# Performance work log

Hardware: AMD Instinct MI355X
Metric: run time of the kernel (lower is better)

Reference implementation:

```python
import jax, jax.numpy as jnp
import numpy as np

N_FFT = 512
HOP = 128
WIN = 512
Q = 0.1
PCT_WIN = 31
FREQ_WIN = 5
TIME_WIN = 9
STRENGTH = 0.35
THRESH = 1.5
TEMP = 0.15
MIN_MASK = 0.08


def _hann_periodic(n):
    # matches torch.hann_window(n) (periodic)
    return (0.5 * (1.0 - jnp.cos(2.0 * jnp.pi * jnp.arange(n) / n))).astype(jnp.float32)


def _stft(x, window):
    # x: (B, L) -> complex (B, F, T); center=True, reflect pad
    pad = N_FFT // 2
    xp = jnp.pad(x, ((0, 0), (pad, pad)), mode='reflect')
    T = 1 + (xp.shape[-1] - N_FFT) // HOP
    idx = (jnp.arange(T) * HOP)[:, None] + jnp.arange(N_FFT)  # (T, n_fft)
    frames = xp[:, idx] * window  # (B, T, n_fft)
    return jnp.fft.rfft(frames, axis=-1).transpose(0, 2, 1)  # (B, F, T)


def _istft(spec, window, length):
    # spec: (B, F, T) complex -> (B, length)
    frames = jnp.fft.irfft(spec.transpose(0, 2, 1), n=N_FFT, axis=-1) * window  # (B,T,n_fft)
    B, T, _ = frames.shape
    total = N_FFT + HOP * (T - 1)
    idx = ((jnp.arange(T) * HOP)[:, None] + jnp.arange(N_FFT)).ravel()
    out = jnp.zeros((B, total), frames.dtype).at[:, idx].add(frames.reshape(B, -1))
    wsq = jnp.zeros((total,), frames.dtype).at[idx].add(
        jnp.broadcast_to(window ** 2, (T, N_FFT)).ravel())
    out = out / jnp.maximum(wsq, 1e-11)
    pad = N_FFT // 2
    return out[:, pad:pad + length]


def _rolling_quantile(mag):
    # mag: (B, F, T); replicate pad + sliding window of PCT_WIN along time
    p = PCT_WIN // 2
    padded = jnp.pad(mag, ((0, 0), (0, 0), (p, p)), mode='edge')
    T = mag.shape[-1]
    windows = jnp.stack([padded[..., i:i + T] for i in range(PCT_WIN)], axis=-1)  # (B,F,T,W)
    return jnp.quantile(windows, Q, axis=-1)


def _avg_pool(x, k, axis):
    # stride-1 avg pool with zero pad k//2, count_include_pad=True (torch default)
    if k <= 1:
        return x
    p = k // 2
    pads = [(0, 0)] * x.ndim
    pads[axis] = (p, p)
    xp = jnp.pad(x, pads)
    n = x.shape[axis]
    acc = 0.0
    for i in range(k):
        sl = [slice(None)] * x.ndim
        sl[axis] = slice(i, i + n)
        acc = acc + xp[tuple(sl)]
    return acc / k


def setup_inputs() -> dict:
    key = jax.random.key(0)
    k1, k2 = jax.random.split(key)
    B, L = 16, 160000
    noisy = jax.random.normal(k1, (B, L), dtype=jnp.float32)
    enhanced = jax.random.normal(k2, (B, L), dtype=jnp.float32)
    return {"noisy": noisy, "enhanced": enhanced}


def reference(noisy, enhanced):
    length = enhanced.shape[-1]
    window = _hann_periodic(WIN)
    e_spec = _stft(enhanced, window)
    n_spec = _stft(noisy, window)
    e_mag = jnp.maximum(jnp.abs(e_spec), 1e-6)
    n_mag = jnp.maximum(jnp.abs(n_spec), 1e-6)
    # mode == 'sg_input_floor': source is the noisy magnitude
    floor = _rolling_quantile(n_mag)
    floor = _avg_pool(floor, FREQ_WIN, axis=-2)
    floor = _avg_pool(floor, TIME_WIN, axis=-1)
    floor = jnp.maximum(floor, 1e-6)
    mask = jax.nn.sigmoid((e_mag - THRESH * floor) / (TEMP * floor + 1e-6))
    final_mask = MIN_MASK + (1.0 - MIN_MASK) * (1.0 - STRENGTH + STRENGTH * mask)
    phase = e_spec / jnp.maximum(jnp.abs(e_spec), 1e-12)  # unit-phase, = polar(1, angle)
    gated_spec = (e_mag * final_mask).astype(jnp.float32) * phase
    return _istft(gated_spec, window, length)
```

## Files before the change

### kernel.cpp

```cpp
#include <hip/hip_runtime.h>
#include <hip/hip_bf16.h>
#include <math.h>

#define BATCH 16
#define LEN   160000
#define NFFT  512
#define HOP   128
#define NT    1251
#define NF    257
#define PADC  256
#define TWO_PI 6.28318530717958647692f
#define P(i) ((i) + ((i) >> 5))
#define FBUF 528
#define GSTR 264

__device__ __forceinline__ int reflect_idx(int j) {
    j = j < 0 ? -j : j;
    j = j >= LEN ? 2*LEN - 2 - j : j;
    return j;
}

__device__ __forceinline__ float hann(int n) {
    return 0.5f - 0.5f * __cosf(TWO_PI * (float)n * (1.0f / 512.0f));
}

__device__ __forceinline__ __hip_bfloat162 pack_bf2(float x, float y) {
    __hip_bfloat162 r; r.x = __float2bfloat16(x); r.y = __float2bfloat16(y); return r;
}
__device__ __forceinline__ float2 unpack_bf2(__hip_bfloat162 v) {
    return make_float2(__bfloat162float(v.x), __bfloat162float(v.y));
}

struct T4 { float m0, m1, m2, m3; };

__device__ __forceinline__ void ins(T4& a, float v) {
    const float x0 = fminf(a.m0, v);  const float c0 = fmaxf(a.m0, v);
    const float x1 = fminf(a.m1, c0); const float c1 = fmaxf(a.m1, c0);
    const float x2 = fminf(a.m2, c1); const float c2 = fmaxf(a.m2, c1);
    const float x3 = fminf(a.m3, c2);
    a.m0 = x0; a.m1 = x1; a.m2 = x2; a.m3 = x3;
}

__device__ __forceinline__ T4 sort4(float a, float b, float c, float d) {
    const float x0 = fminf(a, b), x1 = fmaxf(a, b);
    const float x2 = fminf(c, d), x3 = fmaxf(c, d);
    const float y0 = fminf(x0, x2), y2 = fmaxf(x0, x2);
    const float y1 = fminf(x1, x3), y3 = fmaxf(x1, x3);
    T4 r; r.m0 = y0; r.m1 = fminf(y1, y2); r.m2 = fmaxf(y1, y2); r.m3 = y3;
    return r;
}

__device__ __forceinline__ float merge4_m3(const T4& a, const T4& b) {
    const float l0 = fminf(a.m0, b.m3);
    const float l1 = fminf(a.m1, b.m2);
    const float l2 = fminf(a.m2, b.m1);
    const float l3 = fminf(a.m3, b.m0);
    return fmaxf(fmaxf(l0, l1), fmaxf(l2, l3));
}

__device__ __forceinline__ void dft8(float vr[8], float vi[8], float sign) {
    const float K = 0.70710678118654752f;
    float ar=vr[0]+vr[4], ai=vi[0]+vi[4];
    float br=vr[0]-vr[4], bi=vi[0]-vi[4];
    float cr=vr[2]+vr[6], ci=vi[2]+vi[6];
    float dr=vr[2]-vr[6], di=vi[2]-vi[6];
    float er=vr[1]+vr[5], ei=vi[1]+vi[5];
    float fr=vr[1]-vr[5], fi=vi[1]-vi[5];
    float gr=vr[3]+vr[7], gi=vi[3]+vi[7];
    float hr=vr[3]-vr[7], hi=vi[3]-vi[7];
    const float W4dr = -sign*di, W4di = sign*dr;
    const float W4hr = -sign*hi, W4hi = sign*hr;
    const float E0r=ar+cr, E0i=ai+ci, E2r=ar-cr, E2i=ai-ci;
    const float E1r=br+W4dr, E1i=bi+W4di, E3r=br-W4dr, E3i=bi-W4di;
    const float O0r=er+gr, O0i=ei+gi, O2r=er-gr, O2i=ei-gi;
    const float O1r=fr+W4hr, O1i=fi+W4hi, O3r=fr-W4hr, O3i=fi-W4hi;
    const float T1r = K*(O1r - sign*O1i), T1i = K*(O1i + sign*O1r);
    const float T2r = -sign*O2i,          T2i = sign*O2r;
    const float T3r = K*(-O3r - sign*O3i), T3i = K*(-O3i + sign*O3r);
    vr[0]=E0r+O0r; vi[0]=E0i+O0i;  vr[4]=E0r-O0r; vi[4]=E0i-O0i;
    vr[1]=E1r+T1r; vi[1]=E1i+T1i;  vr[5]=E1r-T1r; vi[5]=E1i-T1i;
    vr[2]=E2r+T2r; vi[2]=E2i+T2i;  vr[6]=E2r-T2r; vi[6]=E2i-T2i;
    vr[3]=E3r+T3r; vi[3]=E3i+T3i;  vr[7]=E3r-T3r; vi[7]=E3i-T3i;
}

template<int NS>
__device__ __forceinline__ void fft_pass(float* R, float* I, int j, float sign) {
    float vr[8], vi[8];
    #pragma unroll
    for (int r = 0; r < 8; ++r) { vr[r] = R[P(j + 64*r)]; vi[r] = I[P(j + 64*r)]; }
    const float th = sign * (TWO_PI / (8.0f * (float)NS)) * (float)(j & (NS - 1));
    float w1r, w1i; __sincosf(th, &w1i, &w1r);
    float wr = w1r, wi = w1i;
    #pragma unroll
    for (int r = 1; r < 8; ++r) {
        const float tr = vr[r]*wr - vi[r]*wi;
        vi[r] = vr[r]*wi + vi[r]*wr; vr[r] = tr;
        const float nwr = wr*w1r - wi*w1i;
        wi = wr*w1i + wi*w1r; wr = nwr;
    }
    dft8(vr, vi, sign);
    const int base = ((j / NS) * (8 * NS)) + (j & (NS - 1));
    #pragma unroll
    for (int r = 0; r < 8; ++r) { R[P(base + r*NS)] = vr[r]; I[P(base + r*NS)] = vi[r]; }
}

__device__ __forceinline__ void fft_pass_last(const float* R, const float* I, int j,
                                              float sign, float vr[8], float vi[8]) {
    #pragma unroll
    for (int r = 0; r < 8; ++r) { vr[r] = R[P(j + 64*r)]; vi[r] = I[P(j + 64*r)]; }
    const float th = sign * (TWO_PI / 512.0f) * (float)j;
    float w1r, w1i; __sincosf(th, &w1i, &w1r);
    float wr = w1r, wi = w1i;
    #pragma unroll
    for (int r = 1; r < 8; ++r) {
        const float tr = vr[r]*wr - vi[r]*wi;
        vi[r] = vr[r]*wi + vi[r]*wr; vr[r] = tr;
        const float nwr = wr*w1r - wi*w1i;
        wi = wr*w1i + wi*w1r; wr = nwr;
    }
    dft8(vr, vi, sign);
}

__global__ __launch_bounds__(256, 6) void stft_kernel(const float* __restrict__ enh,
                                                      const float* __restrict__ noi,
                                                      __hip_bfloat162* __restrict__ e_spec,
                                                      __hip_bfloat16*  __restrict__ n_mag,
                                                      float* __restrict__ out) {
    __shared__ float Ar[4*FBUF], Ai[4*FBUF];
    const int tid = threadIdx.x;
    const int w = tid >> 6, j = tid & 63;
    const int tr_ = blockIdx.x * 4 + w;
    const bool live = tr_ < NT;
    const int t = live ? tr_ : NT - 1;
    const int b = blockIdx.y;
    float* ar = Ar + w*FBUF; float* ai = Ai + w*FBUF;

    {
        const int z = (blockIdx.x << 9) + (tid << 1);
        if (z < LEN) *reinterpret_cast<float2*>(out + (size_t)b * LEN + z) = make_float2(0.0f, 0.0f);
    }

    {
        const int sbase = t * HOP - PADC;
        float vr[8], vi[8];
        if (sbase >= 0 && sbase + NFFT <= LEN) {
            const float* __restrict__ pe = enh + b * LEN + sbase;
            const float* __restrict__ pn = noi + b * LEN + sbase;
            #pragma unroll
            for (int r = 0; r < 8; ++r) {
                const int n = j + 64*r;
                const float wd = hann(n);
                vr[r] = pe[n] * wd;
                vi[r] = pn[n] * wd;
            }
        } else {
            const float* __restrict__ pe = enh + b * LEN;
            const float* __restrict__ pn = noi + b * LEN;
            #pragma unroll
            for (int r = 0; r < 8; ++r) {
                const int n = j + 64*r;
                const int idx = reflect_idx(sbase + n);
                const float wd = hann(n);
                vr[r] = pe[idx] * wd;
                vi[r] = pn[idx] * wd;
            }
        }
        dft8(vr, vi, -1.0f);
        #pragma unroll
        for (int r = 0; r < 8; ++r) { ar[P(8*j + r)] = vr[r]; ai[P(8*j + r)] = vi[r]; }
    }
    fft_pass<8>(ar, ai, j, -1.0f);
    float zr[8], zi[8];
    fft_pass_last(ar, ai, j, -1.0f, zr, zi);

    const int src = (64 - j) & 63;
    float pr[4], pi_[4];
    #pragma unroll
    for (int q = 4; q < 8; ++q) {
        pr[q-4]  = __shfl(zr[q], src);
        pi_[q-4] = __shfl(zi[q], src);
    }
    if (live) {
        const int obase = (b * NT + t) * NF;
        #pragma unroll
        for (int r = 0; r < 4; ++r) {
            const int kk = j + 64*r;
            const float yr = (j == 0) ? zr[(8 - r) & 7] : pr[3 - r];
            const float yi = (j == 0) ? zi[(8 - r) & 7] : pi_[3 - r];
            const float er = 0.5f*(zr[r] + yr), ei = 0.5f*(zi[r] - yi);
            const float nr = 0.5f*(zi[r] + yi), ni = 0.5f*(yr - zr[r]);
            e_spec[obase + kk] = pack_bf2(er, ei);
            n_mag[obase + kk] = __float2bfloat16(fmaxf(sqrtf(nr*nr + ni*ni), 1e-6f));
        }
        if (j == 0) {
            e_spec[obase + 256] = pack_bf2(zr[4], 0.0f);
            n_mag[obase + 256] = __float2bfloat16(fmaxf(fabsf(zi[4]), 1e-6f));
        }
    }
}

__global__ __launch_bounds__(256, 4) void floor_mask_istft_kernel(
        const __hip_bfloat162* __restrict__ g,
        const __hip_bfloat16* __restrict__ n_mag,
        float* __restrict__ out) {
    __shared__ float smem[16 * GSTR];
    __shared__ float fq[16];
    float (*q)[GSTR] = reinterpret_cast<float (*)[GSTR]>(smem);
    float* gr = smem;
    float* gi = smem + 8 * GSTR;

    const int tid = threadIdx.x;
    const int w = tid >> 6, j = tid & 63;
    const int t0 = blockIdx.x * 8, b = blockIdx.y;
    const __hip_bfloat16* __restrict__ pb = n_mag + b * NT * NF;

    {
        const int f = tid;
        float wa[16];
        #pragma unroll
        for (int r = 0; r < 16; ++r) {
            int tr = t0 - 19 + r;
            tr = tr < 0 ? 0 : (tr > NT - 1 ? NT - 1 : tr);
            wa[r] = __bfloat162float(pb[tr * NF + f]);
        }
        T4 s[16];
        s[15].m0 = wa[15]; s[15].m1 = 3.4e38f; s[15].m2 = 3.4e38f; s[15].m3 = 3.4e38f;
        #pragma unroll
        for (int k = 14; k >= 0; --k) { s[k] = s[k+1]; ins(s[k], wa[k]); }
        float wc[15];
        #pragma unroll
        for (int r = 0; r < 15; ++r) {
            int tr = t0 - 3 + r;
            tr = tr < 0 ? 0 : (tr > NT - 1 ? NT - 1 : tr);
            wc[r] = __bfloat162float(pb[tr * NF + f]);
        }
        T4 p = sort4(wc[0], wc[1], wc[2], wc[3]);
        #pragma unroll
        for (int r = 4; r < 15; ++r) ins(p, wc[r]);
        float wb[15];
        #pragma unroll
        for (int r = 0; r < 15; ++r) {
            int tr = t0 + 12 + r;
            tr = tr < 0 ? 0 : (tr > NT - 1 ? NT - 1 : tr);
            wb[r] = __bfloat162float(pb[tr * NF + f]);
        }
        #pragma unroll
        for (int k = 0; k < 16; ++k) {
            q[k][f] = merge4_m3(s[k], p);
            if (k < 15) ins(p, wb[k]);
        }
    }
    if (tid < 16) {
        const int k = tid;
        T4 m; m.m0 = m.m1 = m.m2 = m.m3 = 3.4e38f;
        for (int dt = -15; dt <= 15; ++dt) {
            int tt = t0 - 4 + k + dt;
            tt = tt < 0 ? 0 : (tt > NT - 1 ? NT - 1 : tt);
            ins(m, __bfloat162float(pb[tt * NF + 256]));
        }
        q[k][256] = m.m3;
    }
    __syncthreads();

    float fp[16];
    {
        const int f = tid;
        #pragma unroll
        for (int k = 0; k < 16; ++k) {
            float acc = 0.0f;
            #pragma unroll
            for (int df = -2; df <= 2; ++df) {
                const int ff = f + df;
                if (ff >= 0 && ff < NF) acc += q[k][ff];
            }
            fp[k] = acc * (1.0f / 5.0f);
        }
    }
    if (tid < 16) fq[tid] = (q[tid][254] + q[tid][255] + q[tid][256]) * (1.0f / 5.0f);
    __syncthreads();

    float flv[8];
    {
        #pragma unroll
        for (int k = 0; k < 16; ++k) {
            const int tq = t0 - 4 + k;
            fp[k] = (tq >= 0 && tq < NT) ? fp[k] : 0.0f;
        }
        float acc = 0.0f;
        #pragma unroll
        for (int k = 0; k < 9; ++k) acc += fp[k];
        #pragma unroll
        for (int to = 0; to < 8; ++to) {
            flv[to] = fmaxf(acc * (1.0f / 9.0f), 1e-6f);
            if (to < 7) acc += fp[to + 9] - fp[to];
        }
    }

    {
        const int f = tid;
        #pragma unroll
        for (int ft = 0; ft < 8; ++ft) {
            const int t = t0 + ft;
            float grv = 0.0f, giv = 0.0f;
            if (t < NT) {
                const float fl = flv[ft];
                const float2 e2 = unpack_bf2(g[(b * NT + t) * NF + f]);
                const float a = sqrtf(e2.x * e2.x + e2.y * e2.y);
                const float emag = fmaxf(a, 1e-6f);
                const float xarg = (emag - 1.5f * fl) / (0.15f * fl + 1e-6f);
                const float mask = 1.0f / (1.0f + __expf(-xarg));
                const float fm = 0.08f + 0.92f * (0.65f + 0.35f * mask);
                const float scale = emag * fm / fmaxf(a, 1e-12f);
                grv = e2.x * scale; giv = e2.y * scale;
            }
            gr[ft * GSTR + f] = grv;
            gi[ft * GSTR + f] = giv;
        }
    }
    if (tid < 8) {
        const int ft = tid;
        const int t = t0 + ft;
        float grv = 0.0f, giv = 0.0f;
        if (t < NT) {
            float acc = 0.0f;
            #pragma unroll
            for (int k = 0; k < 9; ++k) {
                const int tq = t0 - 4 + ft + k;
                acc += (tq >= 0 && tq < NT) ? fq[ft + k] : 0.0f;
            }
            const float fl = fmaxf(acc * (1.0f / 9.0f), 1e-6f);
            const float2 e2 = unpack_bf2(g[(b * NT + t) * NF + 256]);
            const float a = sqrtf(e2.x * e2.x + e2.y * e2.y);
            const float emag = fmaxf(a, 1e-6f);
            const float xarg = (emag - 1.5f * fl) / (0.15f * fl + 1e-6f);
            const float mask = 1.0f / (1.0f + __expf(-xarg));
            const float fm = 0.08f + 0.92f * (0.65f + 0.35f * mask);
            const float scale = emag * fm / fmaxf(a, 1e-12f);
            grv = e2.x * scale; giv = e2.y * scale;
        }
        gr[ft * GSTR + 256] = grv;
        gi[ft * GSTR + 256] = giv;
    }
    __syncthreads();

    float* g0r = gr + (2*w) * GSTR;      float* g0i = gi + (2*w) * GSTR;
    float* g1r = gr + (2*w + 1) * GSTR;  float* g1i = gi + (2*w + 1) * GSTR;
    float* ar = g0r;
    float* ai = g0i;

    {
        float vr[8], vi[8];
        #pragma unroll
        for (int r = 0; r < 8; ++r) {
            const int n = j + 64*r;
            float cr, ci;
            if (n <= 256) {
                cr = g0r[n] - g1i[n];
                ci = g0i[n] + g1r[n];
            } else {
                const int m = 512 - n;
                cr = g0r[m] + g1i[m];
                ci = g1r[m] - g0i[m];
            }
            vr[r] = cr; vi[r] = ci;
        }
        dft8(vr, vi, 1.0f);
        #pragma unroll
        for (int r = 0; r < 8; ++r) { ar[P(8*j + r)] = vr[r]; ai[P(8*j + r)] = vi[r]; }
    }
    fft_pass<8>(ar, ai, j, 1.0f);
    float xr[8], xi[8];
    fft_pass_last(ar, ai, j, 1.0f, xr, xi);

    #pragma unroll
    for (int r = 0; r < 8; ++r) {
        const int n = j + 64*r;
        const float wd = hann(n) * (1.0f / 512.0f);
        ar[P(n)] = xr[r] * wd;
        ai[P(n)] = xi[r] * wd;
    }
    __syncthreads();

    const int i0 = t0 << 7;
    for (int s = tid; s < 1408; s += 256) {
        const int i = i0 + s;
        const int jj = i - PADC;
        if (jj < 0 || jj >= LEN) continue;
        const int tl = (i >= 384) ? ((i - 384) >> 7) : 0;
        int th = i >> 7; if (th > NT - 1) th = NT - 1;
        const int ca = tl > t0 ? tl : t0;
        const int cb = th < t0 + 7 ? th : t0 + 7;
        if (cb < ca) continue;
        float acc = 0.0f;
        for (int t = ca; t <= cb; ++t) {
            const int ft = t - t0;
            const int n = i - (t << 7);
            acc += ((ft & 1) ? gi : gr)[(ft >> 1) * FBUF + P(n)];
        }
        float winv;
        if (th - tl == 3) winv = (2.0f / 3.0f);
        else {
            float wacc = 0.0f;
            for (int t = tl; t <= th; ++t) {
                const float wd = hann(i - (t << 7));
                wacc += wd * wd;
            }
            winv = 1.0f / fmaxf(wacc, 1e-11f);
        }
        const float v = acc * winv;
        if (tl >= t0 && th <= t0 + 7) out[b * LEN + jj] = v;
        else atomicAdd(out + b * LEN + jj, v);
    }
}

extern "C" void kernel_launch(void* const* d_in, const int* in_sizes, int n_in,
                              void* d_out, int out_size, void* d_ws, size_t ws_size,
                              hipStream_t stream) {
    const float* noisy    = (const float*)d_in[0];
    const float* enhanced = (const float*)d_in[1];
    float* out = (float*)d_out;

    float* ws = (float*)d_ws;
    __hip_bfloat162* e_spec = (__hip_bfloat162*)ws;
    __hip_bfloat16* n_mag = (__hip_bfloat16*)(ws + 5144112);

    stft_kernel<<<dim3((NT + 3) / 4, BATCH), dim3(256), 0, stream>>>(enhanced, noisy, e_spec, n_mag, out);
    floor_mask_istft_kernel<<<dim3((NT + 7) / 8, BATCH), dim3(256), 0, stream>>>(e_spec, n_mag, out);
}
```

Before: 128.7 us.

## Pack rolling quantile as u16 pairs, reorder pooling, fast-math intrinsics, interior fast paths

The rolling 31-tap quantile now runs on raw bf16 bit patterns as packed 16-bit integer pairs, so two output frames share each min/max instruction, and it reuses a loaded ring of samples instead of three separate window loads. The time average pool is now applied in registers before the frequency pool, which removes one shared-memory pass and one barrier. Division and sqrt are replaced with AMD hardware rcp/sqrt builtins. Interior blocks take unclamped fast paths for both the quantile loads and the overlap-add, skipping bounds checks and window-sum recomputation. Unsigned-integer ordering on bf16 bits is only valid for non-negative magnitudes, and the approximate rcp/sqrt add small error.

Measured after the change: 122.5 us. 1.05x faster.

```diff
diff --git a/kernel.cpp b/kernel.cpp
--- a/kernel.cpp
+++ b/kernel.cpp
@@ -14,6 +14,9 @@
 #define FBUF 528
 #define GSTR 264
 
+__device__ __forceinline__ float rcpf(float x)  { return __builtin_amdgcn_rcpf(x); }
+__device__ __forceinline__ float sqrtf_fast(float x) { return __builtin_amdgcn_sqrtf(x); }
+
 __device__ __forceinline__ int reflect_idx(int j) {
     j = j < 0 ? -j : j;
     j = j >= LEN ? 2*LEN - 2 - j : j;
@@ -41,21 +44,41 @@
     a.m0 = x0; a.m1 = x1; a.m2 = x2; a.m3 = x3;
 }
 
-__device__ __forceinline__ T4 sort4(float a, float b, float c, float d) {
-    const float x0 = fminf(a, b), x1 = fmaxf(a, b);
-    const float x2 = fminf(c, d), x3 = fmaxf(c, d);
-    const float y0 = fminf(x0, x2), y2 = fmaxf(x0, x2);
-    const float y1 = fminf(x1, x3), y3 = fmaxf(x1, x3);
-    T4 r; r.m0 = y0; r.m1 = fminf(y1, y2); r.m2 = fmaxf(y1, y2); r.m3 = y3;
+typedef unsigned short u16t;
+typedef u16t us2 __attribute__((ext_vector_type(2)));
+
+__device__ __forceinline__ us2 mk2(u16t lo, u16t hi) { us2 v; v.x = lo; v.y = hi; return v; }
+__device__ __forceinline__ us2 pmin(us2 a, us2 b) { return __builtin_elementwise_min(a, b); }
+__device__ __forceinline__ us2 pmax(us2 a, us2 b) { return __builtin_elementwise_max(a, b); }
+__device__ __forceinline__ float bfbits2f(u16t x) {
+    return __uint_as_float(((unsigned int)x) << 16);
+}
+
+struct PT4 { us2 m0, m1, m2, m3; };
+
+__device__ __forceinline__ void insP(PT4& a, us2 v) {
+    const us2 x0 = pmin(a.m0, v);  const us2 c0 = pmax(a.m0, v);
+    const us2 x1 = pmin(a.m1, c0); const us2 c1 = pmax(a.m1, c0);
+    const us2 x2 = pmin(a.m2, c1); const us2 c2 = pmax(a.m2, c1);
+    const us2 x3 = pmin(a.m3, c2);
+    a.m0 = x0; a.m1 = x1; a.m2 = x2; a.m3 = x3;
+}
+
+__device__ __forceinline__ PT4 sort4P(us2 a, us2 b, us2 c, us2 d) {
+    const us2 x0 = pmin(a, b), x1 = pmax(a, b);
+    const us2 x2 = pmin(c, d), x3 = pmax(c, d);
+    const us2 y0 = pmin(x0, x2), y2 = pmax(x0, x2);
+    const us2 y1 = pmin(x1, x3), y3 = pmax(x1, x3);
+    PT4 r; r.m0 = y0; r.m1 = pmin(y1, y2); r.m2 = pmax(y1, y2); r.m3 = y3;
     return r;
 }
 
-__device__ __forceinline__ float merge4_m3(const T4& a, const T4& b) {
-    const float l0 = fminf(a.m0, b.m3);
-    const float l1 = fminf(a.m1, b.m2);
-    const float l2 = fminf(a.m2, b.m1);
-    const float l3 = fminf(a.m3, b.m0);
-    return fmaxf(fmaxf(l0, l1), fmaxf(l2, l3));
+__device__ __forceinline__ us2 merge4_m3P(const PT4& a, const PT4& b) {
+    const us2 l0 = pmin(a.m0, b.m3);
+    const us2 l1 = pmin(a.m1, b.m2);
+    const us2 l2 = pmin(a.m2, b.m1);
+    const us2 l3 = pmin(a.m3, b.m0);
+    return pmax(pmax(l0, l1), pmax(l2, l3));
 }
 
 __device__ __forceinline__ void dft8(float vr[8], float vi[8], float sign) {
@@ -190,12 +213,69 @@
             const float er = 0.5f*(zr[r] + yr), ei = 0.5f*(zi[r] - yi);
             const float nr = 0.5f*(zi[r] + yi), ni = 0.5f*(yr - zr[r]);
             e_spec[obase + kk] = pack_bf2(er, ei);
-            n_mag[obase + kk] = __float2bfloat16(fmaxf(sqrtf(nr*nr + ni*ni), 1e-6f));
+            n_mag[obase + kk] = __float2bfloat16(fmaxf(sqrtf_fast(nr*nr + ni*ni), 1e-6f));
         }
         if (j == 0) {
             e_spec[obase + 256] = pack_bf2(zr[4], 0.0f);
             n_mag[obase + 256] = __float2bfloat16(fmaxf(fabsf(zi[4]), 1e-6f));
         }
+    }
+}
+
+template<bool CL>
+__device__ __forceinline__ void phaseQP(const u16t* __restrict__ pbu,
+                                        int t0, int f, float qv[16]) {
+    const us2 PINF = mk2((u16t)0xFFFFu, (u16t)0xFFFFu);
+    u16t wlo[16];
+    #pragma unroll
+    for (int r = 0; r < 16; ++r) {
+        int tr = t0 - 19 + r;
+        if (CL) { tr = tr < 0 ? 0 : (tr > NT - 1 ? NT - 1 : tr); }
+        wlo[r] = pbu[tr * NF + f];
+    }
+    PT4 S[8];
+    S[7].m0 = mk2(wlo[7], wlo[15]);
+    S[7].m1 = S[7].m2 = S[7].m3 = PINF;
+    #pragma unroll
+    for (int k = 6; k >= 0; --k) { S[k] = S[k+1]; insP(S[k], mk2(wlo[k], wlo[k+8])); }
+    u16t ring[8];
+    #pragma unroll
+    for (int i = 0; i < 8; ++i) ring[i] = wlo[8 + i];
+    PT4 Pp;
+    {
+        us2 Wt[4];
+        #pragma unroll
+        for (int r = 8; r < 12; ++r) {
+            int tr = t0 - 19 + r + 8;
+            if (CL) { tr = tr < 0 ? 0 : (tr > NT - 1 ? NT - 1 : tr); }
+            const u16t hi = pbu[tr * NF + f];
+            Wt[r - 8] = mk2(ring[r & 7], hi);
+            ring[r & 7] = hi;
+        }
+        Pp = sort4P(Wt[0], Wt[1], Wt[2], Wt[3]);
+    }
+    #pragma unroll
+    for (int r = 12; r < 31; ++r) {
+        int tr = t0 - 19 + r + 8;
+        if (CL) { tr = tr < 0 ? 0 : (tr > NT - 1 ? NT - 1 : tr); }
+        const u16t hi = pbu[tr * NF + f];
+        insP(Pp, mk2(ring[r & 7], hi));
+        ring[r & 7] = hi;
+    }
+    {
+        const us2 m = merge4_m3P(S[0], Pp);
+        qv[0] = bfbits2f(m.x); qv[8] = bfbits2f(m.y);
+    }
+    #pragma unroll
+    for (int k = 1; k < 8; ++k) {
+        const int r = 30 + k;
+        int tr = t0 - 19 + r + 8;
+        if (CL) { tr = tr < 0 ? 0 : (tr > NT - 1 ? NT - 1 : tr); }
+        const u16t hi = pbu[tr * NF + f];
+        insP(Pp, mk2(ring[r & 7], hi));
+        ring[r & 7] = hi;
+        const us2 m = merge4_m3P(S[k], Pp);
+        qv[k] = bfbits2f(m.x); qv[8 + k] = bfbits2f(m.y);
     }
 }
 
@@ -204,8 +284,7 @@
         const __hip_bfloat16* __restrict__ n_mag,
         float* __restrict__ out) {
     __shared__ float smem[16 * GSTR];
-    __shared__ float fq[16];
-    float (*q)[GSTR] = reinterpret_cast<float (*)[GSTR]>(smem);
+    float* TPl = smem;
     float* gr = smem;
     float* gi = smem + 8 * GSTR;
 
@@ -213,41 +292,28 @@
     const int w = tid >> 6, j = tid & 63;
     const int t0 = blockIdx.x * 8, b = blockIdx.y;
     const __hip_bfloat16* __restrict__ pb = n_mag + b * NT * NF;
-
-    {
-        const int f = tid;
-        float wa[16];
-        #pragma unroll
-        for (int r = 0; r < 16; ++r) {
-            int tr = t0 - 19 + r;
-            tr = tr < 0 ? 0 : (tr > NT - 1 ? NT - 1 : tr);
-            wa[r] = __bfloat162float(pb[tr * NF + f]);
-        }
-        T4 s[16];
-        s[15].m0 = wa[15]; s[15].m1 = 3.4e38f; s[15].m2 = 3.4e38f; s[15].m3 = 3.4e38f;
-        #pragma unroll
-        for (int k = 14; k >= 0; --k) { s[k] = s[k+1]; ins(s[k], wa[k]); }
-        float wc[15];
-        #pragma unroll
-        for (int r = 0; r < 15; ++r) {
-            int tr = t0 - 3 + r;
-            tr = tr < 0 ? 0 : (tr > NT - 1 ? NT - 1 : tr);
-            wc[r] = __bfloat162float(pb[tr * NF + f]);
-        }
-        T4 p = sort4(wc[0], wc[1], wc[2], wc[3]);
-        #pragma unroll
-        for (int r = 4; r < 15; ++r) ins(p, wc[r]);
-        float wb[15];
-        #pragma unroll
-        for (int r = 0; r < 15; ++r) {
-            int tr = t0 + 12 + r;
-            tr = tr < 0 ? 0 : (tr > NT - 1 ? NT - 1 : tr);
-            wb[r] = __bfloat162float(pb[tr * NF + f]);
-        }
+    const u16t* __restrict__ pbu = (const u16t*)pb;
+    const int f = tid;
+
+    float qv[16];
+    if (t0 >= 19 && t0 + 26 <= NT - 1) {
+        phaseQP<false>(pbu, t0, f, qv);
+    } else {
+        phaseQP<true>(pbu, t0, f, qv);
         #pragma unroll
         for (int k = 0; k < 16; ++k) {
-            q[k][f] = merge4_m3(s[k], p);
-            if (k < 15) ins(p, wb[k]);
+            const int tq = t0 - 4 + k;
+            if (tq < 0 || tq >= NT) qv[k] = 0.0f;
+        }
+    }
+    {
+        float acc = 0.0f;
+        #pragma unroll
+        for (int k = 0; k < 9; ++k) acc += qv[k];
+        #pragma unroll
+        for (int to = 0; to < 8; ++to) {
+            TPl[to * GSTR + f] = acc * (1.0f / 9.0f);
+            if (to < 7) acc += qv[to + 9] - qv[to];
         }
     }
     if (tid < 16) {
@@ -258,59 +324,48 @@
             tt = tt < 0 ? 0 : (tt > NT - 1 ? NT - 1 : tt);
             ins(m, __bfloat162float(pb[tt * NF + 256]));
         }
-        q[k][256] = m.m3;
+        float qk = m.m3;
+        const int tq = t0 - 4 + k;
+        if (tq < 0 || tq >= NT) qk = 0.0f;
+        float acc = 0.0f;
+        #pragma unroll
+        for (int d = 0; d < 9; ++d) acc += __shfl(qk, k + d);
+        if (tid < 8) TPl[tid * GSTR + 256] = acc * (1.0f / 9.0f);
     }
     __syncthreads();
 
-    float fp[16];
-    {
-        const int f = tid;
-        #pragma unroll
-        for (int k = 0; k < 16; ++k) {
-            float acc = 0.0f;
-            #pragma unroll
-            for (int df = -2; df <= 2; ++df) {
-                const int ff = f + df;
-                if (ff >= 0 && ff < NF) acc += q[k][ff];
-            }
-            fp[k] = acc * (1.0f / 5.0f);
-        }
-    }
-    if (tid < 16) fq[tid] = (q[tid][254] + q[tid][255] + q[tid][256]) * (1.0f / 5.0f);
+    float fl[8];
+    #pragma unroll
+    for (int to = 0; to < 8; ++to) {
+        float acc = 0.0f;
+        #pragma unroll
+        for (int df = -2; df <= 2; ++df) {
+            const int ff = f + df;
+            if (ff >= 0 && ff < NF) acc += TPl[to * GSTR + ff];
+        }
+        fl[to] = fmaxf(acc * (1.0f / 5.0f), 1e-6f);
+    }
+    float fl256 = 0.0f;
+    if (tid < 8) {
+        fl256 = fmaxf((TPl[tid * GSTR + 254] + TPl[tid * GSTR + 255] +
+                       TPl[tid * GSTR + 256]) * (1.0f / 5.0f), 1e-6f);
+    }
     __syncthreads();
 
-    float flv[8];
-    {
-        #pragma unroll
-        for (int k = 0; k < 16; ++k) {
-            const int tq = t0 - 4 + k;
-            fp[k] = (tq >= 0 && tq < NT) ? fp[k] : 0.0f;
-        }
-        float acc = 0.0f;
-        #pragma unroll
-        for (int k = 0; k < 9; ++k) acc += fp[k];
-        #pragma unroll
-        for (int to = 0; to < 8; ++to) {
-            flv[to] = fmaxf(acc * (1.0f / 9.0f), 1e-6f);
-            if (to < 7) acc += fp[to + 9] - fp[to];
-        }
-    }
-
-    {
-        const int f = tid;
+    {
         #pragma unroll
         for (int ft = 0; ft < 8; ++ft) {
             const int t = t0 + ft;
             float grv = 0.0f, giv = 0.0f;
             if (t < NT) {
-                const float fl = flv[ft];
+                const float flv = fl[ft];
                 const float2 e2 = unpack_bf2(g[(b * NT + t) * NF + f]);
-                const float a = sqrtf(e2.x * e2.x + e2.y * e2.y);
+                const float a = sqrtf_fast(e2.x * e2.x + e2.y * e2.y);
                 const float emag = fmaxf(a, 1e-6f);
-                const float xarg = (emag - 1.5f * fl) / (0.15f * fl + 1e-6f);
-                const float mask = 1.0f / (1.0f + __expf(-xarg));
+                const float xarg = (emag - 1.5f * flv) * rcpf(0.15f * flv + 1e-6f);
+                const float mask = rcpf(1.0f + __expf(-xarg));
                 const float fm = 0.08f + 0.92f * (0.65f + 0.35f * mask);
-                const float scale = emag * fm / fmaxf(a, 1e-12f);
+                const float scale = emag * fm * rcpf(fmaxf(a, 1e-12f));
                 grv = e2.x * scale; giv = e2.y * scale;
             }
             gr[ft * GSTR + f] = grv;
@@ -322,20 +377,14 @@
         const int t = t0 + ft;
         float grv = 0.0f, giv = 0.0f;
         if (t < NT) {
-            float acc = 0.0f;
-            #pragma unroll
-            for (int k = 0; k < 9; ++k) {
-                const int tq = t0 - 4 + ft + k;
-                acc += (tq >= 0 && tq < NT) ? fq[ft + k] : 0.0f;
-            }
-            const float fl = fmaxf(acc * (1.0f / 9.0f), 1e-6f);
+            const float flv = fl256;
             const float2 e2 = unpack_bf2(g[(b * NT + t) * NF + 256]);
-            const float a = sqrtf(e2.x * e2.x + e2.y * e2.y);
+            const float a = sqrtf_fast(e2.x * e2.x + e2.y * e2.y);
             const float emag = fmaxf(a, 1e-6f);
-            const float xarg = (emag - 1.5f * fl) / (0.15f * fl + 1e-6f);
-            const float mask = 1.0f / (1.0f + __expf(-xarg));
+            const float xarg = (emag - 1.5f * flv) * rcpf(0.15f * flv + 1e-6f);
+            const float mask = rcpf(1.0f + __expf(-xarg));
             const float fm = 0.08f + 0.92f * (0.65f + 0.35f * mask);
-            const float scale = emag * fm / fmaxf(a, 1e-12f);
+            const float scale = emag * fm * rcpf(fmaxf(a, 1e-12f));
             grv = e2.x * scale; giv = e2.y * scale;
         }
         gr[ft * GSTR + 256] = grv;
@@ -382,34 +431,54 @@
     __syncthreads();
 
     const int i0 = t0 << 7;
-    for (int s = tid; s < 1408; s += 256) {
-        const int i = i0 + s;
-        const int jj = i - PADC;
-        if (jj < 0 || jj >= LEN) continue;
-        const int tl = (i >= 384) ? ((i - 384) >> 7) : 0;
-        int th = i >> 7; if (th > NT - 1) th = NT - 1;
-        const int ca = tl > t0 ? tl : t0;
-        const int cb = th < t0 + 7 ? th : t0 + 7;
-        if (cb < ca) continue;
-        float acc = 0.0f;
-        for (int t = ca; t <= cb; ++t) {
-            const int ft = t - t0;
-            const int n = i - (t << 7);
-            acc += ((ft & 1) ? gi : gr)[(ft >> 1) * FBUF + P(n)];
-        }
-        float winv;
-        if (th - tl == 3) winv = (2.0f / 3.0f);
-        else {
-            float wacc = 0.0f;
-            for (int t = tl; t <= th; ++t) {
-                const float wd = hann(i - (t << 7));
-                wacc += wd * wd;
-            }
-            winv = 1.0f / fmaxf(wacc, 1e-11f);
-        }
-        const float v = acc * winv;
-        if (tl >= t0 && th <= t0 + 7) out[b * LEN + jj] = v;
-        else atomicAdd(out + b * LEN + jj, v);
+    if (t0 >= 3 && t0 + 10 <= NT - 1) {
+        for (int s = tid; s < 1408; s += 256) {
+            const int i = i0 + s;
+            const int tl = (i - 384) >> 7;
+            const int th = tl + 3;
+            const int ca = tl > t0 ? tl : t0;
+            const int cb = th < t0 + 7 ? th : t0 + 7;
+            float acc = 0.0f;
+            for (int t = ca; t <= cb; ++t) {
+                const int ft = t - t0;
+                const int n = i - (t << 7);
+                acc += ((ft & 1) ? gi : gr)[(ft >> 1) * FBUF + P(n)];
+            }
+            const float v = acc * (2.0f / 3.0f);
+            const int jj = i - PADC;
+            if (tl >= t0 && th <= t0 + 7) out[b * LEN + jj] = v;
+            else atomicAdd(out + b * LEN + jj, v);
+        }
+    } else {
+        for (int s = tid; s < 1408; s += 256) {
+            const int i = i0 + s;
+            const int jj = i - PADC;
+            if (jj < 0 || jj >= LEN) continue;
+            const int tl = (i >= 384) ? ((i - 384) >> 7) : 0;
+            int th = i >> 7; if (th > NT - 1) th = NT - 1;
+            const int ca = tl > t0 ? tl : t0;
+            const int cb = th < t0 + 7 ? th : t0 + 7;
+            if (cb < ca) continue;
+            float acc = 0.0f;
+            for (int t = ca; t <= cb; ++t) {
+                const int ft = t - t0;
+                const int n = i - (t << 7);
+                acc += ((ft & 1) ? gi : gr)[(ft >> 1) * FBUF + P(n)];
+            }
+            float winv;
+            if (th - tl == 3) winv = (2.0f / 3.0f);
+            else {
+                float wacc = 0.0f;
+                for (int t = tl; t <= th; ++t) {
+                    const float wd = hann(i - (t << 7));
+                    wacc += wd * wd;
+                }
+                winv = rcpf(fmaxf(wacc, 1e-11f));
+            }
+            const float v = acc * winv;
+            if (tl >= t0 && th <= t0 + 7) out[b * LEN + jj] = v;
+            else atomicAdd(out + b * LEN + jj, v);
+        }
     }
 }
 
```
